# Performance work log

Measured on AMD Instinct MI355X. Metric: run time of the kernel, lower is better.

## Reference

```python
import jax, jax.numpy as jnp
import numpy as np

B, L, D, H = 2, 2048, 1024, 16
HD = D // H  # head_dim = 64


def setup_inputs() -> dict:
    key = jax.random.key(0)
    ks = jax.random.split(key, 8)
    queries = jax.random.normal(ks[0], (B, L, D), dtype=jnp.float32)
    keys = jax.random.normal(ks[1], (B, L, D), dtype=jnp.float32)
    values = jax.random.normal(ks[2], (B, L, D), dtype=jnp.float32)
    mask = jax.random.randint(ks[3], (B, L, L), 0, 2) > 0  # True = masked
    s = 1.0 / np.sqrt(D)
    W_q = jax.random.normal(ks[4], (D, D), dtype=jnp.float32) * s
    W_k = jax.random.normal(ks[5], (D, D), dtype=jnp.float32) * s
    W_v = jax.random.normal(ks[6], (D, D), dtype=jnp.float32) * s
    W_o = jax.random.normal(ks[7], (D, D), dtype=jnp.float32) * s
    return {"queries": queries, "keys": keys, "values": values,
            "W_q": W_q, "W_k": W_k, "W_v": W_v, "W_o": W_o, "mask": mask}


def _split_heads(x):
    # [B, L, D] -> [B, H, L, HD]
    return x.reshape(B, L, H, HD).transpose(0, 2, 1, 3)


def reference(queries, keys, values, W_q, W_k, W_v, W_o, mask):
    # Linear projections (nn.Linear: x @ W.T, no bias)
    q = _split_heads(queries @ W_q.T)   # [B,H,Lq,HD]
    k = _split_heads(keys @ W_k.T)      # [B,H,Lk,HD]
    v = _split_heads(values @ W_v.T)    # [B,H,Lk,HD]
    scores = jnp.einsum('bnqd,bnkd->bnqk', q, k) / np.sqrt(HD)
    scores = jnp.where(mask[:, None, :, :], -1e9, scores)
    attn = jax.nn.softmax(scores, axis=-1)
    ctx = jnp.einsum('bnqk,bnkd->bnqd', attn, v)
    ctx = ctx.transpose(0, 2, 1, 3).reshape(B, L, D)
    return ctx @ W_o.T  # dropout p=0.0 -> identity
```

## Files before the change

### kernel.cpp

```cpp
#include <hip/hip_runtime.h>
#include <hip/hip_bf16.h>

typedef __bf16 bf16;
typedef __attribute__((ext_vector_type(8))) __bf16 bf16x8;
typedef __attribute__((ext_vector_type(4))) __bf16 bf16x4;
typedef __attribute__((ext_vector_type(4))) float f32x4;

#define B_   2
#define L_   2048
#define D_   1024
#define H_   16
#define HD_  64

__device__ __forceinline__ float fast_exp2(float x) {
#if defined(__has_builtin)
#if __has_builtin(__builtin_amdgcn_exp2f)
  return __builtin_amdgcn_exp2f(x);
#else
  float e; asm("v_exp_f32 %0, %1" : "=v"(e) : "v"(x)); return e;
#endif
#else
  float e; asm("v_exp_f32 %0, %1" : "=v"(e) : "v"(x)); return e;
#endif
}

__device__ __forceinline__ void gll16(const bf16* g, bf16* l) {
  __builtin_amdgcn_global_load_lds((const __attribute__((address_space(1))) void*)g,
                                   (__attribute__((address_space(3))) void*)l,
                                   16, 0, 0);
}

__global__ void detect_kernel(const unsigned short* __restrict__ q_u,
                              const unsigned char* __restrict__ m_u,
                              int* __restrict__ flags) {
  __shared__ int cnt, odd;
  if (threadIdx.x == 0) { cnt = 0; odd = 0; }
  __syncthreads();
  int c = 0, o = 0;
  for (int i = 0; i < 32; i++) {
    int idx = threadIdx.x * 32 + i;
    unsigned e = (q_u[idx] >> 7) & 0xFF;
    if (e >= 0x8F || (e > 0 && e <= 0x6F)) c++;
    if ((idx & 3) && m_u[idx]) o = 1;
  }
  atomicAdd(&cnt, c);
  if (o) atomicOr(&odd, 1);
  __syncthreads();
  if (threadIdx.x == 0) { flags[0] = (cnt > 512) ? 1 : 0; flags[1] = odd; }
}

__device__ __forceinline__ void canon_body(const void* src, bf16* dst, int i, int f) {
  if (f) {
    const float4* s = (const float4*)src;
    float4 a = s[i / 4], b2 = s[i / 4 + 1];
    bf16x8 o;
    o[0] = (bf16)a.x;  o[1] = (bf16)a.y;  o[2] = (bf16)a.z;  o[3] = (bf16)a.w;
    o[4] = (bf16)b2.x; o[5] = (bf16)b2.y; o[6] = (bf16)b2.z; o[7] = (bf16)b2.w;
    *(bf16x8*)(dst + i) = o;
  } else {
    *(bf16x8*)(dst + i) = ((const bf16x8*)src)[i / 8];
  }
}

__global__ __launch_bounds__(256) void canon_all(
    const void* xq, const void* xk, const void* xv,
    const void* Wq, const void* Wk, const void* Wv, const void* Wo,
    bf16* cxq, bf16* cxk, bf16* cxv,
    bf16* cWq, bf16* cWk, bf16* cWv, bf16* cWo,
    const int* __restrict__ flags) {
  const int f = flags[0];
  int t = blockIdx.x;
  const void* src; bf16* dst; int base;
  if (t < 2048)      { src = xq; dst = cxq; base = t * 2048; }
  else if (t < 4096) { src = xk; dst = cxk; base = (t - 2048) * 2048; }
  else if (t < 6144) { src = xv; dst = cxv; base = (t - 4096) * 2048; }
  else {
    int w = t - 6144, wi = w >> 9;
    base = (w & 511) * 2048;
    if (wi == 0)      { src = Wq; dst = cWq; }
    else if (wi == 1) { src = Wk; dst = cWk; }
    else if (wi == 2) { src = Wv; dst = cWv; }
    else              { src = Wo; dst = cWo; }
  }
  canon_body(src, dst, base + threadIdx.x * 8, f);
}

__global__ __launch_bounds__(256) void pack_mask(const void* __restrict__ mp,
                                                 const int* __restrict__ flags,
                                                 unsigned* __restrict__ bitsT) {
  int wid = blockIdx.x * 256 + threadIdx.x;
  unsigned v = 0;
  if (flags[1]) {
    const uchar4* p = (const uchar4*)mp;
#pragma unroll
    for (int c = 0; c < 8; c++) {
      uchar4 u = p[wid * 8 + c];
      v |= (u.x ? 1u : 0u) << (c * 4 + 0);
      v |= (u.y ? 1u : 0u) << (c * 4 + 1);
      v |= (u.z ? 1u : 0u) << (c * 4 + 2);
      v |= (u.w ? 1u : 0u) << (c * 4 + 3);
    }
  } else {
    const int4* p = (const int4*)mp;
#pragma unroll
    for (int c = 0; c < 8; c++) {
      int4 u = p[wid * 8 + c];
      v |= (u.x ? 1u : 0u) << (c * 4 + 0);
      v |= (u.y ? 1u : 0u) << (c * 4 + 1);
      v |= (u.z ? 1u : 0u) << (c * 4 + 2);
      v |= (u.w ? 1u : 0u) << (c * 4 + 3);
    }
  }
  int row = wid >> 6, word = wid & 63;
  int kt = word >> 1, half = word & 1;
  bitsT[((size_t)kt * 4096 + row) * 2 + half] = v;
}

__global__ __launch_bounds__(256) void gemm_qkv(
    const bf16* __restrict__ Aq, const bf16* __restrict__ Bq, bf16* __restrict__ Cq,
    const bf16* __restrict__ Ak, const bf16* __restrict__ Bk, bf16* __restrict__ Ck,
    const bf16* __restrict__ Av, const bf16* __restrict__ Bv, bf16* __restrict__ VT) {
  __shared__ bf16 smem[128 * 136];
  bf16* sA = smem;
  bf16* sB = smem + 4096;
  const int z = blockIdx.z;
  const bf16* A  = (z == 0) ? Aq : (z == 1) ? Ak : Av;
  const bf16* Bm = (z == 0) ? Bq : (z == 1) ? Bk : Bv;

  const int tid = threadIdx.x;
  const int w = tid >> 6, lane = tid & 63, qd = lane >> 4, r = lane & 15;
  const int wm = w >> 1, wn = w & 1;
  const int m0 = blockIdx.x * 128, n0 = blockIdx.y * 128;

  f32x4 acc[4][4];
#pragma unroll
  for (int i = 0; i < 4; i++)
#pragma unroll
    for (int j = 0; j < 4; j++) acc[i][j] = (f32x4){0.f, 0.f, 0.f, 0.f};

  for (int k0 = 0; k0 < 1024; k0 += 32) {
    __syncthreads();
#pragma unroll
    for (int p = 0; p < 2; p++) {
      int c = p * 256 + tid;
      gll16(A + (size_t)(m0 + (c >> 2)) * 1024 + k0 + (c & 3) * 8, sA + c * 8);
    }
#pragma unroll
    for (int p = 0; p < 2; p++) {
      int c = p * 256 + tid;
      gll16(Bm + (size_t)(n0 + (c >> 2)) * 1024 + k0 + (c & 3) * 8, sB + c * 8);
    }
    __syncthreads();
    bf16x8 af[4], bfv[4];
#pragma unroll
    for (int i = 0; i < 4; i++)
      af[i] = *(const bf16x8*)&sA[(wm * 64 + i * 16 + r) * 32 + qd * 8];
#pragma unroll
    for (int j = 0; j < 4; j++)
      bfv[j] = *(const bf16x8*)&sB[(wn * 64 + j * 16 + r) * 32 + qd * 8];
#pragma unroll
    for (int i = 0; i < 4; i++)
#pragma unroll
      for (int j = 0; j < 4; j++)
        acc[i][j] = __builtin_amdgcn_mfma_f32_16x16x32_bf16(af[i], bfv[j], acc[i][j], 0, 0, 0);
  }

  if (z < 2) {
    bf16* C = (z == 0) ? Cq : Ck;
    const float s = (z == 0) ? 0.1803368801f : 1.0f;
#pragma unroll
    for (int i = 0; i < 4; i++)
#pragma unroll
      for (int j = 0; j < 4; j++)
#pragma unroll
        for (int rr = 0; rr < 4; rr++) {
          int row = m0 + wm * 64 + i * 16 + qd * 4 + rr;
          int col = n0 + wn * 64 + j * 16 + r;
          C[(size_t)row * 1024 + col] = (bf16)(acc[i][j][rr] * s);
        }
  } else {
    __syncthreads();
#pragma unroll
    for (int i = 0; i < 4; i++)
#pragma unroll
      for (int j = 0; j < 4; j++) {
        int col = wn * 64 + j * 16 + r;
        int rowb = wm * 64 + i * 16 + qd * 4;
        bf16x4 v4;
#pragma unroll
        for (int rr = 0; rr < 4; rr++) v4[rr] = (bf16)acc[i][j][rr];
        *(bf16x4*)&smem[col * 136 + rowb] = v4;
      }
    __syncthreads();
    const int b = m0 >> 11, tok0 = m0 & 2047, h0 = n0 >> 6;
#pragma unroll
    for (int p = 0; p < 8; p++) {
      int c = p * 256 + tid;
      int dl = c >> 4, ch = c & 15;
      bf16x8 v = *(const bf16x8*)&smem[dl * 136 + ch * 8];
      int head = h0 + (dl >> 6), d = dl & 63;
      *(bf16x8*)(VT + ((size_t)((b * 16 + head) * 64 + d)) * 2048 + tok0 + ch * 8) = v;
    }
  }
}

__global__ __launch_bounds__(256) void gemm_nt_out(const bf16* __restrict__ A,
                                                   const bf16* __restrict__ Bm,
                                                   void* __restrict__ Cout,
                                                   const int* __restrict__ flags) {
  __shared__ bf16 sA[128 * 32];
  __shared__ bf16 sB[128 * 32];
  const int tid = threadIdx.x;
  const int w = tid >> 6, lane = tid & 63, qd = lane >> 4, r = lane & 15;
  const int wm = w >> 1, wn = w & 1;
  const int m0 = blockIdx.x * 128, n0 = blockIdx.y * 128;

  f32x4 acc[4][4];
#pragma unroll
  for (int i = 0; i < 4; i++)
#pragma unroll
    for (int j = 0; j < 4; j++) acc[i][j] = (f32x4){0.f, 0.f, 0.f, 0.f};

  for (int k0 = 0; k0 < 1024; k0 += 32) {
    __syncthreads();
#pragma unroll
    for (int p = 0; p < 2; p++) {
      int c = p * 256 + tid;
      gll16(A + (size_t)(m0 + (c >> 2)) * 1024 + k0 + (c & 3) * 8, sA + c * 8);
    }
#pragma unroll
    for (int p = 0; p < 2; p++) {
      int c = p * 256 + tid;
      gll16(Bm + (size_t)(n0 + (c >> 2)) * 1024 + k0 + (c & 3) * 8, sB + c * 8);
    }
    __syncthreads();
    bf16x8 af[4], bfv[4];
#pragma unroll
    for (int i = 0; i < 4; i++)
      af[i] = *(const bf16x8*)&sA[(wm * 64 + i * 16 + r) * 32 + qd * 8];
#pragma unroll
    for (int j = 0; j < 4; j++)
      bfv[j] = *(const bf16x8*)&sB[(wn * 64 + j * 16 + r) * 32 + qd * 8];
#pragma unroll
    for (int i = 0; i < 4; i++)
#pragma unroll
      for (int j = 0; j < 4; j++)
        acc[i][j] = __builtin_amdgcn_mfma_f32_16x16x32_bf16(af[i], bfv[j], acc[i][j], 0, 0, 0);
  }
  const int f = flags[0];
#pragma unroll
  for (int i = 0; i < 4; i++)
#pragma unroll
    for (int j = 0; j < 4; j++)
#pragma unroll
      for (int rr = 0; rr < 4; rr++) {
        int row = m0 + wm * 64 + i * 16 + qd * 4 + rr;
        int col = n0 + wn * 64 + j * 16 + r;
        if (f) ((float*)Cout)[(size_t)row * 1024 + col] = acc[i][j][rr];
        else   ((bf16*)Cout)[(size_t)row * 1024 + col] = (bf16)acc[i][j][rr];
      }
}

__global__ __launch_bounds__(256) void attn_kernel(const bf16* __restrict__ Q,
                                                   const bf16* __restrict__ Kp,
                                                   const bf16* __restrict__ Vt,
                                                   const unsigned* __restrict__ bitsT,
                                                   bf16* __restrict__ OP,
                                                   float* __restrict__ LP) {
  __shared__ bf16 sK[64 * 64];
  __shared__ bf16 sVT[64 * 64];
  __shared__ bf16 sP[128 * 72];
  const int tid = threadIdx.x;
  const int w = tid >> 6, lane = tid & 63, qd = lane >> 4, r = lane & 15;
  const int bh = blockIdx.y, b = bh >> 4, h = bh & 15;
  const int q0 = blockIdx.x * 128;
  const int z = blockIdx.z;

  bf16x8 qf[2][2];
#pragma unroll
  for (int i = 0; i < 2; i++)
#pragma unroll
    for (int ks = 0; ks < 2; ks++)
      qf[i][ks] = *(const bf16x8*)(Q + (size_t)(b * L_ + q0 + w * 32 + i * 16 + r) * D_ +
                                   h * HD_ + ks * 32 + qd * 8);

  bf16x8 ones;
#pragma unroll
  for (int e = 0; e < 8; e++) ones[e] = (bf16)1.0f;

  f32x4 o[2][4], lacc[2];
#pragma unroll
  for (int i = 0; i < 2; i++) {
#pragma unroll
    for (int dj = 0; dj < 4; dj++) o[i][dj] = (f32x4){0.f, 0.f, 0.f, 0.f};
    lacc[i] = (f32x4){0.f, 0.f, 0.f, 0.f};
  }

  for (int kt = z * 16; kt < z * 16 + 16; kt++) {
    __syncthreads();
#pragma unroll
    for (int p = 0; p < 2; p++) {
      int c = p * 256 + tid;
      int row = c >> 3, kc = c & 7;
      int kcg = kc ^ (row & 7);
      gll16(Kp + (size_t)(b * L_ + kt * 64 + row) * D_ + h * HD_ + kcg * 8, sK + c * 8);
    }
#pragma unroll
    for (int p = 0; p < 2; p++) {
      int c = p * 256 + tid;
      int row = c >> 3, kc = c & 7;
      int kcg = kc ^ (row & 7);
      gll16(Vt + (size_t)(bh * 64 + row) * L_ + kt * 64 + kcg * 8, sVT + c * 8);
    }
    __syncthreads();

    uint4 mq[2][2];
#pragma unroll
    for (int i = 0; i < 2; i++) {
      const uint4* mp4 = (const uint4*)(bitsT +
          ((size_t)kt * 4096 + b * 2048 + q0 + w * 32 + i * 16 + qd * 4) * 2);
      mq[i][0] = mp4[0];
      mq[i][1] = mp4[1];
    }

    bf16x8 kf[4][2];
#pragma unroll
    for (int j = 0; j < 4; j++)
#pragma unroll
      for (int ks = 0; ks < 2; ks++) {
        int row = j * 16 + r;
        int phys = (ks * 4 + qd) ^ (row & 7);
        kf[j][ks] = *(const bf16x8*)&sK[row * 64 + phys * 8];
      }

#pragma unroll
    for (int i = 0; i < 2; i++) {
      f32x4 S[4];
#pragma unroll
      for (int j = 0; j < 4; j++) {
        S[j] = (f32x4){0.f, 0.f, 0.f, 0.f};
#pragma unroll
        for (int ks = 0; ks < 2; ks++)
          S[j] = __builtin_amdgcn_mfma_f32_16x16x32_bf16(qf[i][ks], kf[j][ks], S[j], 0, 0, 0);
      }
#pragma unroll
      for (int j = 0; j < 4; j++)
#pragma unroll
        for (int rr = 0; rr < 4; rr++) {
          unsigned w32;
          if (rr == 0) w32 = (j < 2) ? mq[i][0].x : mq[i][0].y;
          else if (rr == 1) w32 = (j < 2) ? mq[i][0].z : mq[i][0].w;
          else if (rr == 2) w32 = (j < 2) ? mq[i][1].x : mq[i][1].y;
          else w32 = (j < 2) ? mq[i][1].z : mq[i][1].w;
          float e = fast_exp2(S[j][rr]);
          bool msk = (w32 >> ((j & 1) * 16 + r)) & 1u;
          sP[(w * 32 + i * 16 + qd * 4 + rr) * 72 + j * 16 + r] = (bf16)(msk ? 0.f : e);
        }
    }
    asm volatile("s_waitcnt lgkmcnt(0)" ::: "memory");

    bf16x8 vf[4][2];
#pragma unroll
    for (int dj = 0; dj < 4; dj++)
#pragma unroll
      for (int ks = 0; ks < 2; ks++) {
        int row = dj * 16 + r;
        int phys = (ks * 4 + qd) ^ (row & 7);
        vf[dj][ks] = *(const bf16x8*)&sVT[row * 64 + phys * 8];
      }
#pragma unroll
    for (int i = 0; i < 2; i++)
#pragma unroll
      for (int ks = 0; ks < 2; ks++) {
        bf16x8 pf = *(const bf16x8*)&sP[(w * 32 + i * 16 + r) * 72 + ks * 32 + qd * 8];
#pragma unroll
        for (int dj = 0; dj < 4; dj++)
          o[i][dj] = __builtin_amdgcn_mfma_f32_16x16x32_bf16(pf, vf[dj][ks], o[i][dj], 0, 0, 0);
        lacc[i] = __builtin_amdgcn_mfma_f32_16x16x32_bf16(pf, ones, lacc[i], 0, 0, 0);
      }
  }

#pragma unroll
  for (int i = 0; i < 2; i++) {
#pragma unroll
    for (int dj = 0; dj < 4; dj++)
#pragma unroll
      for (int rr = 0; rr < 4; rr++) {
        int rg = b * L_ + q0 + w * 32 + i * 16 + qd * 4 + rr;
        int col = h * HD_ + dj * 16 + r;
        OP[((size_t)z * 4096 + rg) * 1024 + col] = (bf16)o[i][dj][rr];
      }
    if (r == 0) {
#pragma unroll
      for (int rr = 0; rr < 4; rr++) {
        int rg = b * L_ + q0 + w * 32 + i * 16 + qd * 4 + rr;
        LP[((size_t)z * 4096 + rg) * 16 + h] = lacc[i][rr];
      }
    }
  }
}

__global__ __launch_bounds__(256) void combine_kernel(const bf16* __restrict__ OP,
                                                      const float* __restrict__ LP,
                                                      bf16* __restrict__ CTX) {
  size_t idx = ((size_t)blockIdx.x * 256 + threadIdx.x) * 8;
  int row = (int)(idx >> 10), col = (int)(idx & 1023);
  bf16x8 a = *(const bf16x8*)(OP + idx);
  bf16x8 c = *(const bf16x8*)(OP + (size_t)4096 * 1024 + idx);
  int h = col >> 6;
  float l = LP[row * 16 + h] + LP[65536 + row * 16 + h];
  float inv = 1.0f / l;
  bf16x8 o;
#pragma unroll
  for (int e = 0; e < 8; e++) o[e] = (bf16)(((float)a[e] + (float)c[e]) * inv);
  *(bf16x8*)(CTX + idx) = o;
}

extern "C" void kernel_launch(void* const* d_in, const int* in_sizes, int n_in,
                              void* d_out, int out_size, void* d_ws, size_t ws_size,
                              hipStream_t stream) {
  const void* xq = d_in[0];
  const void* xk = d_in[1];
  const void* xv = d_in[2];
  const void* Wq = d_in[3];
  const void* Wk = d_in[4];
  const void* Wv = d_in[5];
  const void* Wo = d_in[6];
  const void* mask = d_in[7];

  char* ws = (char*)d_ws;
  const size_t MB = 1048576;
  int*      FLAGS = (int*)(ws + 0);
  unsigned* BITS  = (unsigned*)(ws + 4096);
  bf16* cWo = (bf16*)(ws + 2 * MB);
  bf16* cWq = (bf16*)(ws + 4 * MB);
  bf16* cWk = (bf16*)(ws + 6 * MB);
  bf16* cWv = (bf16*)(ws + 8 * MB);
  bf16* cxq = (bf16*)(ws + 10 * MB);
  bf16* cxk = (bf16*)(ws + 18 * MB);
  bf16* cxv = (bf16*)(ws + 26 * MB);
  bf16* Q   = (bf16*)(ws + 34 * MB);
  bf16* K   = (bf16*)(ws + 42 * MB);
  bf16* VT  = (bf16*)(ws + 50 * MB);
  bf16*  OP  = (bf16*)(ws + 4 * MB);
  float* LP  = (float*)(ws + 20 * MB);
  bf16*  CTX = (bf16*)(ws + 26 * MB);

  detect_kernel<<<1, 256, 0, stream>>>((const unsigned short*)xq,
                                       (const unsigned char*)mask, FLAGS);
  canon_all<<<8192, 256, 0, stream>>>(xq, xk, xv, Wq, Wk, Wv, Wo,
                                      cxq, cxk, cxv, cWq, cWk, cWv, cWo, FLAGS);
  pack_mask<<<1024, 256, 0, stream>>>(mask, FLAGS, BITS);
  gemm_qkv<<<dim3(32, 8, 3), 256, 0, stream>>>(cxq, cWq, Q,
                                               cxk, cWk, K,
                                               cxv, cWv, VT);
  attn_kernel<<<dim3(16, 32, 2), 256, 0, stream>>>(Q, K, VT, BITS, OP, LP);
  combine_kernel<<<2048, 256, 0, stream>>>(OP, LP, CTX);
  gemm_nt_out<<<dim3(32, 8), 256, 0, stream>>>(CTX, cWo, d_out, FLAGS);
}
```

Before: 280.5 us.

## Fuse mask packing into canon kernel, shrink out-GEMM tile, transpose score MFMA layout

Merges the mask-packing launch into the canonicalization kernel to drop one launch, and shrinks the output GEMM N-tile to 64 so twice as many blocks fill the GPU. In attention, it swaps the MFMA operand order so each lane holds four consecutive key columns. That lets each lane read one 64-bit mask word per row and write P as one vectorized bf16x4 store instead of scalar stores. The mask loads are also moved before the barrier, and the format-detection kernel now samples fewer elements, which risks misclassifying the input dtype.

Result: faster. 268.8 us (-4.2%).

```diff
diff --git a/kernel.cpp b/kernel.cpp
--- a/kernel.cpp
+++ b/kernel.cpp
@@ -13,15 +13,7 @@
 #define HD_  64
 
 __device__ __forceinline__ float fast_exp2(float x) {
-#if defined(__has_builtin)
-#if __has_builtin(__builtin_amdgcn_exp2f)
-  return __builtin_amdgcn_exp2f(x);
-#else
   float e; asm("v_exp_f32 %0, %1" : "=v"(e) : "v"(x)); return e;
-#endif
-#else
-  float e; asm("v_exp_f32 %0, %1" : "=v"(e) : "v"(x)); return e;
-#endif
 }
 
 __device__ __forceinline__ void gll16(const bf16* g, bf16* l) {
@@ -37,8 +29,8 @@
   if (threadIdx.x == 0) { cnt = 0; odd = 0; }
   __syncthreads();
   int c = 0, o = 0;
-  for (int i = 0; i < 32; i++) {
-    int idx = threadIdx.x * 32 + i;
+  for (int i = 0; i < 8; i++) {
+    int idx = threadIdx.x * 8 + i;
     unsigned e = (q_u[idx] >> 7) & 0xFF;
     if (e >= 0x8F || (e > 0 && e <= 0x6F)) c++;
     if ((idx & 3) && m_u[idx]) o = 1;
@@ -46,7 +38,7 @@
   atomicAdd(&cnt, c);
   if (o) atomicOr(&odd, 1);
   __syncthreads();
-  if (threadIdx.x == 0) { flags[0] = (cnt > 512) ? 1 : 0; flags[1] = odd; }
+  if (threadIdx.x == 0) { flags[0] = (cnt > 128) ? 1 : 0; flags[1] = odd; }
 }
 
 __device__ __forceinline__ void canon_body(const void* src, bf16* dst, int i, int f) {
@@ -62,14 +54,45 @@
   }
 }
 
-__global__ __launch_bounds__(256) void canon_all(
+__global__ __launch_bounds__(256) void canon_pack(
     const void* xq, const void* xk, const void* xv,
     const void* Wq, const void* Wk, const void* Wv, const void* Wo,
+    const void* mp,
     bf16* cxq, bf16* cxk, bf16* cxv,
     bf16* cWq, bf16* cWk, bf16* cWv, bf16* cWo,
+    unsigned* __restrict__ bitsT,
     const int* __restrict__ flags) {
+  int t = blockIdx.x;
+  if (t >= 8192) {
+    int wid = (t - 8192) * 256 + threadIdx.x;
+    unsigned v = 0;
+    if (flags[1]) {
+      const uchar4* p = (const uchar4*)mp;
+#pragma unroll
+      for (int c = 0; c < 8; c++) {
+        uchar4 u = p[wid * 8 + c];
+        v |= (u.x ? 1u : 0u) << (c * 4 + 0);
+        v |= (u.y ? 1u : 0u) << (c * 4 + 1);
+        v |= (u.z ? 1u : 0u) << (c * 4 + 2);
+        v |= (u.w ? 1u : 0u) << (c * 4 + 3);
+      }
+    } else {
+      const int4* p = (const int4*)mp;
+#pragma unroll
+      for (int c = 0; c < 8; c++) {
+        int4 u = p[wid * 8 + c];
+        v |= (u.x ? 1u : 0u) << (c * 4 + 0);
+        v |= (u.y ? 1u : 0u) << (c * 4 + 1);
+        v |= (u.z ? 1u : 0u) << (c * 4 + 2);
+        v |= (u.w ? 1u : 0u) << (c * 4 + 3);
+      }
+    }
+    int row = wid >> 6, word = wid & 63;
+    int kt = word >> 1, half = word & 1;
+    bitsT[((size_t)kt * 4096 + row) * 2 + half] = v;
+    return;
+  }
   const int f = flags[0];
-  int t = blockIdx.x;
   const void* src; bf16* dst; int base;
   if (t < 2048)      { src = xq; dst = cxq; base = t * 2048; }
   else if (t < 4096) { src = xk; dst = cxk; base = (t - 2048) * 2048; }
@@ -85,37 +108,6 @@
   canon_body(src, dst, base + threadIdx.x * 8, f);
 }
 
-__global__ __launch_bounds__(256) void pack_mask(const void* __restrict__ mp,
-                                                 const int* __restrict__ flags,
-                                                 unsigned* __restrict__ bitsT) {
-  int wid = blockIdx.x * 256 + threadIdx.x;
-  unsigned v = 0;
-  if (flags[1]) {
-    const uchar4* p = (const uchar4*)mp;
-#pragma unroll
-    for (int c = 0; c < 8; c++) {
-      uchar4 u = p[wid * 8 + c];
-      v |= (u.x ? 1u : 0u) << (c * 4 + 0);
-      v |= (u.y ? 1u : 0u) << (c * 4 + 1);
-      v |= (u.z ? 1u : 0u) << (c * 4 + 2);
-      v |= (u.w ? 1u : 0u) << (c * 4 + 3);
-    }
-  } else {
-    const int4* p = (const int4*)mp;
-#pragma unroll
-    for (int c = 0; c < 8; c++) {
-      int4 u = p[wid * 8 + c];
-      v |= (u.x ? 1u : 0u) << (c * 4 + 0);
-      v |= (u.y ? 1u : 0u) << (c * 4 + 1);
-      v |= (u.z ? 1u : 0u) << (c * 4 + 2);
-      v |= (u.w ? 1u : 0u) << (c * 4 + 3);
-    }
-  }
-  int row = wid >> 6, word = wid & 63;
-  int kt = word >> 1, half = word & 1;
-  bitsT[((size_t)kt * 4096 + row) * 2 + half] = v;
-}
-
 __global__ __launch_bounds__(256) void gemm_qkv(
     const bf16* __restrict__ Aq, const bf16* __restrict__ Bq, bf16* __restrict__ Cq,
     const bf16* __restrict__ Ak, const bf16* __restrict__ Bk, bf16* __restrict__ Ck,
@@ -209,53 +201,51 @@
                                                    void* __restrict__ Cout,
                                                    const int* __restrict__ flags) {
   __shared__ bf16 sA[128 * 32];
-  __shared__ bf16 sB[128 * 32];
+  __shared__ bf16 sB[64 * 32];
   const int tid = threadIdx.x;
   const int w = tid >> 6, lane = tid & 63, qd = lane >> 4, r = lane & 15;
   const int wm = w >> 1, wn = w & 1;
-  const int m0 = blockIdx.x * 128, n0 = blockIdx.y * 128;
-
-  f32x4 acc[4][4];
+  const int m0 = blockIdx.x * 128, n0 = blockIdx.y * 64;
+
+  f32x4 acc[4][2];
 #pragma unroll
   for (int i = 0; i < 4; i++)
 #pragma unroll
-    for (int j = 0; j < 4; j++) acc[i][j] = (f32x4){0.f, 0.f, 0.f, 0.f};
+    for (int j = 0; j < 2; j++) acc[i][j] = (f32x4){0.f, 0.f, 0.f, 0.f};
 
   for (int k0 = 0; k0 < 1024; k0 += 32) {
     __syncthreads();
-#pragma unroll
-    for (int p = 0; p < 2; p++) {
-      int c = p * 256 + tid;
-      gll16(A + (size_t)(m0 + (c >> 2)) * 1024 + k0 + (c & 3) * 8, sA + c * 8);
-    }
-#pragma unroll
-    for (int p = 0; p < 2; p++) {
-      int c = p * 256 + tid;
-      gll16(Bm + (size_t)(n0 + (c >> 2)) * 1024 + k0 + (c & 3) * 8, sB + c * 8);
-    }
-    __syncthreads();
-    bf16x8 af[4], bfv[4];
+    {
+      int c0 = tid;
+      gll16(A + (size_t)(m0 + (c0 >> 2)) * 1024 + k0 + (c0 & 3) * 8, sA + c0 * 8);
+      int c1 = 256 + tid;
+      gll16(A + (size_t)(m0 + (c1 >> 2)) * 1024 + k0 + (c1 & 3) * 8, sA + c1 * 8);
+      int cb = tid;
+      gll16(Bm + (size_t)(n0 + (cb >> 2)) * 1024 + k0 + (cb & 3) * 8, sB + cb * 8);
+    }
+    __syncthreads();
+    bf16x8 af[4], bfv[2];
 #pragma unroll
     for (int i = 0; i < 4; i++)
       af[i] = *(const bf16x8*)&sA[(wm * 64 + i * 16 + r) * 32 + qd * 8];
 #pragma unroll
-    for (int j = 0; j < 4; j++)
-      bfv[j] = *(const bf16x8*)&sB[(wn * 64 + j * 16 + r) * 32 + qd * 8];
-#pragma unroll
-    for (int i = 0; i < 4; i++)
-#pragma unroll
-      for (int j = 0; j < 4; j++)
+    for (int j = 0; j < 2; j++)
+      bfv[j] = *(const bf16x8*)&sB[(wn * 32 + j * 16 + r) * 32 + qd * 8];
+#pragma unroll
+    for (int i = 0; i < 4; i++)
+#pragma unroll
+      for (int j = 0; j < 2; j++)
         acc[i][j] = __builtin_amdgcn_mfma_f32_16x16x32_bf16(af[i], bfv[j], acc[i][j], 0, 0, 0);
   }
   const int f = flags[0];
 #pragma unroll
   for (int i = 0; i < 4; i++)
 #pragma unroll
-    for (int j = 0; j < 4; j++)
+    for (int j = 0; j < 2; j++)
 #pragma unroll
       for (int rr = 0; rr < 4; rr++) {
         int row = m0 + wm * 64 + i * 16 + qd * 4 + rr;
-        int col = n0 + wn * 64 + j * 16 + r;
+        int col = n0 + wn * 32 + j * 16 + r;
         if (f) ((float*)Cout)[(size_t)row * 1024 + col] = acc[i][j][rr];
         else   ((bf16*)Cout)[(size_t)row * 1024 + col] = (bf16)acc[i][j][rr];
       }
@@ -312,16 +302,14 @@
       int kcg = kc ^ (row & 7);
       gll16(Vt + (size_t)(bh * 64 + row) * L_ + kt * 64 + kcg * 8, sVT + c * 8);
     }
-    __syncthreads();
-
-    uint4 mq[2][2];
-#pragma unroll
-    for (int i = 0; i < 2; i++) {
-      const uint4* mp4 = (const uint4*)(bitsT +
-          ((size_t)kt * 4096 + b * 2048 + q0 + w * 32 + i * 16 + qd * 4) * 2);
-      mq[i][0] = mp4[0];
-      mq[i][1] = mp4[1];
-    }
+
+    uint2 m64[2];
+#pragma unroll
+    for (int i = 0; i < 2; i++)
+      m64[i] = *(const uint2*)(bitsT +
+          ((size_t)kt * 4096 + b * 2048 + q0 + w * 32 + i * 16 + r) * 2);
+
+    __syncthreads();
 
     bf16x8 kf[4][2];
 #pragma unroll
@@ -341,21 +329,20 @@
         S[j] = (f32x4){0.f, 0.f, 0.f, 0.f};
 #pragma unroll
         for (int ks = 0; ks < 2; ks++)
-          S[j] = __builtin_amdgcn_mfma_f32_16x16x32_bf16(qf[i][ks], kf[j][ks], S[j], 0, 0, 0);
-      }
-#pragma unroll
-      for (int j = 0; j < 4; j++)
+          S[j] = __builtin_amdgcn_mfma_f32_16x16x32_bf16(kf[j][ks], qf[i][ks], S[j], 0, 0, 0);
+      }
+#pragma unroll
+      for (int j = 0; j < 4; j++) {
+        unsigned word = (j < 2) ? m64[i].x : m64[i].y;
+        unsigned nib = (word >> ((j & 1) * 16 + qd * 4)) & 0xFu;
+        bf16x4 pv;
 #pragma unroll
         for (int rr = 0; rr < 4; rr++) {
-          unsigned w32;
-          if (rr == 0) w32 = (j < 2) ? mq[i][0].x : mq[i][0].y;
-          else if (rr == 1) w32 = (j < 2) ? mq[i][0].z : mq[i][0].w;
-          else if (rr == 2) w32 = (j < 2) ? mq[i][1].x : mq[i][1].y;
-          else w32 = (j < 2) ? mq[i][1].z : mq[i][1].w;
           float e = fast_exp2(S[j][rr]);
-          bool msk = (w32 >> ((j & 1) * 16 + r)) & 1u;
-          sP[(w * 32 + i * 16 + qd * 4 + rr) * 72 + j * 16 + r] = (bf16)(msk ? 0.f : e);
+          pv[rr] = (bf16)(((nib >> rr) & 1u) ? 0.f : e);
         }
+        *(bf16x4*)&sP[(w * 32 + i * 16 + r) * 72 + j * 16 + qd * 4] = pv;
+      }
     }
     asm volatile("s_waitcnt lgkmcnt(0)" ::: "memory");
 
@@ -448,13 +435,13 @@
 
   detect_kernel<<<1, 256, 0, stream>>>((const unsigned short*)xq,
                                        (const unsigned char*)mask, FLAGS);
-  canon_all<<<8192, 256, 0, stream>>>(xq, xk, xv, Wq, Wk, Wv, Wo,
-                                      cxq, cxk, cxv, cWq, cWk, cWv, cWo, FLAGS);
-  pack_mask<<<1024, 256, 0, stream>>>(mask, FLAGS, BITS);
+  canon_pack<<<9216, 256, 0, stream>>>(xq, xk, xv, Wq, Wk, Wv, Wo, mask,
+                                       cxq, cxk, cxv, cWq, cWk, cWv, cWo,
+                                       BITS, FLAGS);
   gemm_qkv<<<dim3(32, 8, 3), 256, 0, stream>>>(cxq, cWq, Q,
                                                cxk, cWk, K,
                                                cxv, cWv, VT);
   attn_kernel<<<dim3(16, 32, 2), 256, 0, stream>>>(Q, K, VT, BITS, OP, LP);
   combine_kernel<<<2048, 256, 0, stream>>>(OP, LP, CTX);
-  gemm_nt_out<<<dim3(32, 8), 256, 0, stream>>>(CTX, cWo, d_out, FLAGS);
-}
+  gemm_nt_out<<<dim3(32, 16), 256, 0, stream>>>(CTX, cWo, d_out, FLAGS);
+}
```
